# Kernel optimization log

Measured on AMD Instinct MI355X. Metric: run time of the kernel, lower is better.

Reference implementation:

```python
import jax, jax.numpy as jnp
import numpy as np

N, E, F_IN, NHID, HEADS, NGRAPHS = 50000, 800000, 128, 256, 4, 16
C = NHID // HEADS          # 64 per-head channels
NEG_SLOPE = 0.2            # PyG GATConv default negative_slope


def setup_inputs() -> dict:
    key = jax.random.key(0)
    k = jax.random.split(key, 7)
    x = jax.random.normal(k[0], (N, F_IN), jnp.float32)
    edge_index = jax.random.randint(k[1], (2, E), 0, N)          # [2, E] src/dst
    batch = jnp.sort(jax.random.randint(k[2], (N,), 0, NGRAPHS))  # node -> graph id
    # learned params of GATConv(F_IN, C, heads=HEADS), concat=True
    W = jax.random.normal(k[3], (F_IN, NHID), jnp.float32) / np.sqrt(F_IN)
    att_src = jax.random.normal(k[4], (HEADS, C), jnp.float32) * 0.1
    att_dst = jax.random.normal(k[5], (HEADS, C), jnp.float32) * 0.1
    bias = jax.random.normal(k[6], (NHID,), jnp.float32) * 0.01
    return {"x": x, "edge_index": edge_index, "batch": batch,
            "W": W, "att_src": att_src, "att_dst": att_dst, "bias": bias}


def _segment_softmax(logits, seg, num_segments):
    # softmax over all edges sharing the same destination node
    m = jax.ops.segment_max(logits, seg, num_segments=num_segments)
    m = jnp.where(jnp.isfinite(m), m, jnp.zeros_like(m))  # guard empty segments
    e = jnp.exp(logits - m[seg])
    s = jax.ops.segment_sum(e, seg, num_segments=num_segments)
    return e / (s[seg] + 1e-16)


def reference(x, edge_index, batch, W, att_src, att_dst, bias):
    n = x.shape[0]
    # PyG GATConv adds self-loops by default
    loops = jnp.arange(n, dtype=edge_index.dtype)
    src = jnp.concatenate([edge_index[0], loops])
    dst = jnp.concatenate([edge_index[1], loops])
    xp = (x @ W).reshape(n, HEADS, C)                       # [N, H, C]
    a_src = jnp.einsum('nhc,hc->nh', xp, att_src)           # [N, H]
    a_dst = jnp.einsum('nhc,hc->nh', xp, att_dst)
    logits = jax.nn.leaky_relu(a_src[src] + a_dst[dst], NEG_SLOPE)  # [E+N, H]
    alpha = _segment_softmax(logits, dst, n)
    msg = xp[src] * alpha[:, :, None]                       # [E+N, H, C]
    out = jax.ops.segment_sum(msg, dst, num_segments=n).reshape(n, NHID) + bias
    h = jax.nn.relu(out)                                    # hidden_act='relu'
    # global max / mean pooling per graph, then concat
    gmax = jax.ops.segment_max(h, batch, num_segments=NGRAPHS)
    cnt = jax.ops.segment_sum(jnp.ones((n, 1), h.dtype), batch, num_segments=NGRAPHS)
    gmean = jax.ops.segment_sum(h, batch, num_segments=NGRAPHS) / (cnt + 1e-16)
    return jnp.concatenate([gmax, gmean], axis=1)           # [NGRAPHS, 2*NHID]
```

## Files before the change

### kernel.cpp

```cpp
#include <hip/hip_runtime.h>

#define NN 50000
#define NE 800000
#define FIN 128
#define NHID 256
#define HEADS 4
#define CPH 64
#define NG 16
#define ETOT (NE + NN)
#define NEG_SLOPE 0.2f
#define MAXDEG 64

__device__ __forceinline__ float lrelu(float x) {
    return x > 0.f ? x : NEG_SLOPE * x;
}
__device__ __forceinline__ unsigned short bf16_rne(float f) {
    unsigned u = __float_as_uint(f);
    unsigned r = (u + 0x7fffu + ((u >> 16) & 1u)) >> 16;
    return (unsigned short)r;
}
__device__ __forceinline__ float bf16_to_f(unsigned short h) {
    return __uint_as_float((unsigned)h << 16);
}
__device__ __forceinline__ float bf16_lo(unsigned u) {
    return __uint_as_float(u << 16);
}
__device__ __forceinline__ float bf16_hi(unsigned u) {
    return __uint_as_float(u & 0xffff0000u);
}

using frag_ab = __attribute__((ext_vector_type(8))) short;
using frag_cd = __attribute__((ext_vector_type(4))) float;

__global__ __launch_bounds__(256) void k_scatter(const int* __restrict__ ei,
                                                 const float* __restrict__ W,
                                                 unsigned short* __restrict__ Wt16,
                                                 int* __restrict__ deg,
                                                 unsigned short* __restrict__ elist) {
    int bid = blockIdx.x;
    if (bid < 128) {
        int idx = bid * 256 + threadIdx.x;
        int n = idx >> 7;
        int k = idx & 127;
        Wt16[idx] = bf16_rne(W[(size_t)k * NHID + n]);
        return;
    }
    int e = (bid - 128) * 256 + threadIdx.x;
    if (e >= ETOT) return;
    int s, d;
    if (e < NE) { s = ei[e]; d = ei[NE + e]; } else { s = d = e - NE; }
    int pos = atomicAdd(&deg[d], 1);
    if (pos < MAXDEG) elist[d * MAXDEG + pos] = (unsigned short)s;
}

__global__ __launch_bounds__(256) void k_gemm(const float* __restrict__ x,
                                              const unsigned short* __restrict__ Wt16,
                                              const float* __restrict__ att_src,
                                              const float* __restrict__ att_dst,
                                              unsigned short* __restrict__ xp16,
                                              float* __restrict__ a_src,
                                              float* __restrict__ a_dst) {
    __shared__ __align__(16) unsigned short smem[64 * 264];
    const int tid = threadIdx.x;
    const int row0 = blockIdx.x * 64;

    {
        int r = tid >> 2;
        int c0 = (tid & 3) * 32;
        int gr = row0 + r;
        if (gr < NN) {
            #pragma unroll
            for (int i = 0; i < 8; i++) {
                float4 v = *(const float4*)&x[(size_t)gr * FIN + c0 + i * 4];
                ushort4 o;
                o.x = bf16_rne(v.x); o.y = bf16_rne(v.y);
                o.z = bf16_rne(v.z); o.w = bf16_rne(v.w);
                *(ushort4*)&smem[r * 264 + c0 + i * 4] = o;
            }
        } else {
            ushort4 z = {0, 0, 0, 0};
            #pragma unroll
            for (int i = 0; i < 8; i++) *(ushort4*)&smem[r * 264 + c0 + i * 4] = z;
        }
    }
    __syncthreads();

    const int wv = tid >> 6;
    const int lane = tid & 63;
    const int rowhalf = wv >> 1;
    const int colhalf = wv & 1;
    const int m = lane & 15;
    const int q = lane >> 4;
    const int cbase = colhalf * 128;

    frag_cd acc[2][8];
    #pragma unroll
    for (int rt = 0; rt < 2; rt++)
        #pragma unroll
        for (int c = 0; c < 8; c++)
            acc[rt][c] = (frag_cd){0.f, 0.f, 0.f, 0.f};

    #pragma unroll
    for (int k0 = 0; k0 < FIN; k0 += 32) {
        frag_ab af0 = *(const frag_ab*)&smem[(rowhalf * 32 + m) * 264 + k0 + q * 8];
        frag_ab af1 = *(const frag_ab*)&smem[(rowhalf * 32 + 16 + m) * 264 + k0 + q * 8];
        #pragma unroll
        for (int c = 0; c < 8; c++) {
            int n = cbase + c * 16 + m;
            frag_ab bf = *(const frag_ab*)&Wt16[(size_t)n * FIN + k0 + q * 8];
            acc[0][c] = __builtin_amdgcn_mfma_f32_16x16x32_bf16(af0, bf, acc[0][c], 0, 0, 0);
            acc[1][c] = __builtin_amdgcn_mfma_f32_16x16x32_bf16(af1, bf, acc[1][c], 0, 0, 0);
        }
    }

    float asv[8], adv[8];
    #pragma unroll
    for (int c = 0; c < 8; c++) {
        asv[c] = att_src[cbase + c * 16 + m];
        adv[c] = att_dst[cbase + c * 16 + m];
    }
    const int headA = colhalf * 2;
    const int headB = colhalf * 2 + 1;

    #pragma unroll
    for (int rt = 0; rt < 2; rt++) {
        #pragma unroll
        for (int reg = 0; reg < 4; reg++) {
            int grow = row0 + rowhalf * 32 + rt * 16 + q * 4 + reg;
            bool ok = grow < NN;
            float psA = 0.f, psB = 0.f, pdA = 0.f, pdB = 0.f;
            #pragma unroll
            for (int c = 0; c < 4; c++) {
                psA += acc[rt][c][reg] * asv[c];
                pdA += acc[rt][c][reg] * adv[c];
                psB += acc[rt][c + 4][reg] * asv[c + 4];
                pdB += acc[rt][c + 4][reg] * adv[c + 4];
            }
            #pragma unroll
            for (int off = 1; off < 16; off <<= 1) {
                psA += __shfl_xor(psA, off, 64);
                psB += __shfl_xor(psB, off, 64);
                pdA += __shfl_xor(pdA, off, 64);
                pdB += __shfl_xor(pdB, off, 64);
            }
            if (m == 0 && ok) {
                a_src[grow * 4 + headA] = psA;
                a_src[grow * 4 + headB] = psB;
                a_dst[grow * 4 + headA] = pdA;
                a_dst[grow * 4 + headB] = pdB;
            }
        }
    }

    __syncthreads();
    #pragma unroll
    for (int rt = 0; rt < 2; rt++)
        #pragma unroll
        for (int c = 0; c < 8; c++)
            #pragma unroll
            for (int reg = 0; reg < 4; reg++)
                smem[(rowhalf * 32 + rt * 16 + q * 4 + reg) * 264 + cbase + c * 16 + m] =
                    bf16_rne(acc[rt][c][reg]);
    __syncthreads();
    {
        int r = tid >> 2;
        int cg = (tid & 3) * 64;
        int gr = row0 + r;
        if (gr < NN) {
            #pragma unroll
            for (int j = 0; j < 2; j++) {
                uint4 v0 = *(const uint4*)&smem[r * 264 + cg + j * 32];
                uint4 v1 = *(const uint4*)&smem[r * 264 + cg + j * 32 + 8];
                uint4 v2 = *(const uint4*)&smem[r * 264 + cg + j * 32 + 16];
                uint4 v3 = *(const uint4*)&smem[r * 264 + cg + j * 32 + 24];
                *(uint4*)&xp16[(size_t)gr * NHID + cg + j * 32] = v0;
                *(uint4*)&xp16[(size_t)gr * NHID + cg + j * 32 + 8] = v1;
                *(uint4*)&xp16[(size_t)gr * NHID + cg + j * 32 + 16] = v2;
                *(uint4*)&xp16[(size_t)gr * NHID + cg + j * 32 + 24] = v3;
            }
        }
    }
}

__global__ __launch_bounds__(256) void k_agg(const unsigned short* __restrict__ elist,
                                             const int* __restrict__ deg,
                                             const float* __restrict__ a_src,
                                             const float* __restrict__ a_dst,
                                             const unsigned short* __restrict__ xp16,
                                             const float* __restrict__ bias,
                                             unsigned short* __restrict__ hbuf16) {
    __shared__ float wlds[4][MAXDEG][4];
    __shared__ int   slds[4][MAXDEG];
    int wv = threadIdx.x >> 6;
    int lane = threadIdx.x & 63;
    int d = blockIdx.x * 4 + wv;
    if (d >= NN) return;
    int dg = deg[d]; if (dg > MAXDEG) dg = MAXDEG;

    float4 ad = *(const float4*)&a_dst[d * 4];

    float4 lg = make_float4(-1e30f, -1e30f, -1e30f, -1e30f);
    if (lane < dg) {
        int s = elist[d * MAXDEG + lane];
        slds[wv][lane] = s;
        float4 as = *(const float4*)&a_src[s * 4];
        lg.x = lrelu(as.x + ad.x);
        lg.y = lrelu(as.y + ad.y);
        lg.z = lrelu(as.z + ad.z);
        lg.w = lrelu(as.w + ad.w);
    }
    float4 m = lg;
    #pragma unroll
    for (int off = 1; off < 64; off <<= 1) {
        m.x = fmaxf(m.x, __shfl_xor(m.x, off, 64));
        m.y = fmaxf(m.y, __shfl_xor(m.y, off, 64));
        m.z = fmaxf(m.z, __shfl_xor(m.z, off, 64));
        m.w = fmaxf(m.w, __shfl_xor(m.w, off, 64));
    }
    float4 w = make_float4(0.f, 0.f, 0.f, 0.f);
    if (lane < dg) {
        w.x = expf(lg.x - m.x);
        w.y = expf(lg.y - m.y);
        w.z = expf(lg.z - m.z);
        w.w = expf(lg.w - m.w);
    }
    *(float4*)&wlds[wv][lane][0] = w;
    float4 sm = w;
    #pragma unroll
    for (int off = 1; off < 64; off <<= 1) {
        sm.x += __shfl_xor(sm.x, off, 64);
        sm.y += __shfl_xor(sm.y, off, 64);
        sm.z += __shfl_xor(sm.z, off, 64);
        sm.w += __shfl_xor(sm.w, off, 64);
    }

    const int half = lane >> 5;
    const int hl = lane & 31;
    const int ch0 = hl * 8;
    const int hh = hl >> 3;
    float denom = (hh == 0 ? sm.x : hh == 1 ? sm.y : hh == 2 ? sm.z : sm.w) + 1e-16f;

    float acc0[8] = {}, acc1[8] = {};
    int e = half;
    for (; e + 2 < dg; e += 4) {
        int sA = slds[wv][e];
        int sB = slds[wv][e + 2];
        float wA = wlds[wv][e][hh];
        float wB = wlds[wv][e + 2][hh];
        uint4 uA = *(const uint4*)&xp16[(size_t)sA * NHID + ch0];
        uint4 uB = *(const uint4*)&xp16[(size_t)sB * NHID + ch0];
        acc0[0] += wA * bf16_lo(uA.x); acc0[1] += wA * bf16_hi(uA.x);
        acc0[2] += wA * bf16_lo(uA.y); acc0[3] += wA * bf16_hi(uA.y);
        acc0[4] += wA * bf16_lo(uA.z); acc0[5] += wA * bf16_hi(uA.z);
        acc0[6] += wA * bf16_lo(uA.w); acc0[7] += wA * bf16_hi(uA.w);
        acc1[0] += wB * bf16_lo(uB.x); acc1[1] += wB * bf16_hi(uB.x);
        acc1[2] += wB * bf16_lo(uB.y); acc1[3] += wB * bf16_hi(uB.y);
        acc1[4] += wB * bf16_lo(uB.z); acc1[5] += wB * bf16_hi(uB.z);
        acc1[6] += wB * bf16_lo(uB.w); acc1[7] += wB * bf16_hi(uB.w);
    }
    if (e < dg) {
        int sA = slds[wv][e];
        float wA = wlds[wv][e][hh];
        uint4 uA = *(const uint4*)&xp16[(size_t)sA * NHID + ch0];
        acc0[0] += wA * bf16_lo(uA.x); acc0[1] += wA * bf16_hi(uA.x);
        acc0[2] += wA * bf16_lo(uA.y); acc0[3] += wA * bf16_hi(uA.y);
        acc0[4] += wA * bf16_lo(uA.z); acc0[5] += wA * bf16_hi(uA.z);
        acc0[6] += wA * bf16_lo(uA.w); acc0[7] += wA * bf16_hi(uA.w);
    }
    #pragma unroll
    for (int j = 0; j < 8; j++) {
        acc0[j] += acc1[j];
        acc0[j] += __shfl_xor(acc0[j], 32, 64);
    }
    if (half == 0) {
        float4 b1 = *(const float4*)&bias[ch0];
        float4 b2 = *(const float4*)&bias[ch0 + 4];
        ushort4 oA, oB;
        oA.x = bf16_rne(fmaxf(acc0[0] / denom + b1.x, 0.f));
        oA.y = bf16_rne(fmaxf(acc0[1] / denom + b1.y, 0.f));
        oA.z = bf16_rne(fmaxf(acc0[2] / denom + b1.z, 0.f));
        oA.w = bf16_rne(fmaxf(acc0[3] / denom + b1.w, 0.f));
        oB.x = bf16_rne(fmaxf(acc0[4] / denom + b2.x, 0.f));
        oB.y = bf16_rne(fmaxf(acc0[5] / denom + b2.y, 0.f));
        oB.z = bf16_rne(fmaxf(acc0[6] / denom + b2.z, 0.f));
        oB.w = bf16_rne(fmaxf(acc0[7] / denom + b2.w, 0.f));
        *(ushort4*)&hbuf16[(size_t)d * NHID + ch0] = oA;
        *(ushort4*)&hbuf16[(size_t)d * NHID + ch0 + 4] = oB;
    }
}

#define NPB 128
__global__ __launch_bounds__(256) void k_pool(const unsigned short* __restrict__ hbuf16,
                                              const int* __restrict__ batch,
                                              float* __restrict__ gmax,
                                              float* __restrict__ gsum) {
    int c = threadIdx.x;
    int n0 = blockIdx.x * NPB;
    if (n0 >= NN) return;
    float lmax = 0.f, lsum = 0.f;
    int cur_g = batch[n0];
    int nend = n0 + NPB; if (nend > NN) nend = NN;
    for (int n = n0; n < nend; n++) {
        int g = batch[n];
        if (g != cur_g) {
            atomicMax((int*)&gmax[cur_g * NHID + c], __float_as_int(lmax));
            atomicAdd(&gsum[cur_g * NHID + c], lsum);
            lmax = 0.f; lsum = 0.f; cur_g = g;
        }
        float val = bf16_to_f(hbuf16[(size_t)n * NHID + c]);
        lmax = fmaxf(lmax, val);
        lsum += val;
    }
    atomicMax((int*)&gmax[cur_g * NHID + c], __float_as_int(lmax));
    atomicAdd(&gsum[cur_g * NHID + c], lsum);
}

__device__ __forceinline__ int lb_batch(const int* __restrict__ batch, int val) {
    int lo = 0, hi = NN;
    while (lo < hi) {
        int mid = (lo + hi) >> 1;
        if (batch[mid] < val) lo = mid + 1; else hi = mid;
    }
    return lo;
}

__global__ __launch_bounds__(512) void k_final(const float* __restrict__ gmax,
                                               const float* __restrict__ gsum,
                                               const int* __restrict__ batch,
                                               float* __restrict__ out) {
    __shared__ float inv_cnt;
    int g = blockIdx.x;
    if (threadIdx.x == 0) {
        int lo = lb_batch(batch, g);
        int hi = lb_batch(batch, g + 1);
        inv_cnt = 1.0f / ((float)(hi - lo) + 1e-16f);
    }
    __syncthreads();
    int j = threadIdx.x;
    float v;
    if (j < 256) v = gmax[g * NHID + j];
    else v = gsum[g * NHID + (j - 256)] * inv_cnt;
    out[g * 512 + j] = v;
}

extern "C" void kernel_launch(void* const* d_in, const int* in_sizes, int n_in,
                              void* d_out, int out_size, void* d_ws, size_t ws_size,
                              hipStream_t stream) {
    const float* x      = (const float*)d_in[0];
    const int*   ei     = (const int*)d_in[1];
    const int*   batch  = (const int*)d_in[2];
    const float* W      = (const float*)d_in[3];
    const float* attS   = (const float*)d_in[4];
    const float* attD   = (const float*)d_in[5];
    const float* bias   = (const float*)d_in[6];
    float* out = (float*)d_out;

    float* ws = (float*)d_ws;
    unsigned short* xp16   = (unsigned short*)ws;
    float*          a_src  = (float*)(xp16 + (size_t)NN * NHID + 256);
    float*          a_dst  = a_src + 200000;
    unsigned short* hbuf16 = (unsigned short*)(a_dst + 200000);
    unsigned short* elist  = hbuf16 + (size_t)NN * NHID;
    int*            deg    = (int*)(elist + (size_t)NN * MAXDEG);
    float*          gmax   = (float*)(deg + NN);
    float*          gsum   = gmax + 4096;
    unsigned short* Wt16   = (unsigned short*)(gsum + 4096);

    size_t zero_bytes = (size_t)(NN + 4096 + 4096) * 4;
    hipMemsetAsync((void*)deg, 0, zero_bytes, stream);

    k_scatter<<<128 + (ETOT + 255) / 256, 256, 0, stream>>>(ei, W, Wt16, deg, elist);
    k_gemm<<<(NN + 63) / 64, 256, 0, stream>>>(x, Wt16, attS, attD, xp16, a_src, a_dst);
    k_agg<<<(NN + 3) / 4, 256, 0, stream>>>(elist, deg, a_src, a_dst, xp16, bias, hbuf16);
    k_pool<<<(NN + NPB - 1) / NPB, 256, 0, stream>>>(hbuf16, batch, gmax, gsum);
    k_final<<<NG, 512, 0, stream>>>(gmax, gsum, batch, out);
}
```

Measured before the change: 273.4 us.

## Fuse scatter, GEMM and zeroing into one front kernel; merge pool and final

Merges the edge-scatter, GEMM and workspace zeroing into one launch, splitting the work by block ID. The GEMM now reads fp32 W directly and converts it to bf16 on the fly, so the separate W transpose pass goes away. Pool and final are merged through a last-block counter with atomic reads. The aggregation softmax drops its max-subtraction, which removes two shuffle reductions but risks exp overflow for large logits. This cuts launches and memsets, but the strided uncoalesced W loads in the GEMM inner loop may cost more than they save.

After: 321.7 us. 17.7% more time.

```diff
diff --git a/kernel.cpp b/kernel.cpp
--- a/kernel.cpp
+++ b/kernel.cpp
@@ -5,12 +5,17 @@
 #define FIN 128
 #define NHID 256
 #define HEADS 4
-#define CPH 64
 #define NG 16
 #define ETOT (NE + NN)
 #define NEG_SLOPE 0.2f
 #define MAXDEG 64
 
+#define ZB 8
+#define NBS ((ETOT + 255) / 256)
+#define NBG ((NN + 63) / 64)
+#define NPB 128
+#define NBP ((NN + NPB - 1) / NPB)
+
 __device__ __forceinline__ float lrelu(float x) {
     return x > 0.f ? x : NEG_SLOPE * x;
 }
@@ -32,37 +37,37 @@
 using frag_ab = __attribute__((ext_vector_type(8))) short;
 using frag_cd = __attribute__((ext_vector_type(4))) float;
 
-__global__ __launch_bounds__(256) void k_scatter(const int* __restrict__ ei,
-                                                 const float* __restrict__ W,
-                                                 unsigned short* __restrict__ Wt16,
-                                                 int* __restrict__ deg,
-                                                 unsigned short* __restrict__ elist) {
-    int bid = blockIdx.x;
-    if (bid < 128) {
-        int idx = bid * 256 + threadIdx.x;
-        int n = idx >> 7;
-        int k = idx & 127;
-        Wt16[idx] = bf16_rne(W[(size_t)k * NHID + n]);
+__global__ __launch_bounds__(256) void k_front(const float* __restrict__ x,
+                                               const float* __restrict__ W,
+                                               const float* __restrict__ att_src,
+                                               const float* __restrict__ att_dst,
+                                               const int* __restrict__ ei,
+                                               int* __restrict__ deg,
+                                               unsigned short* __restrict__ elist,
+                                               unsigned short* __restrict__ xp16,
+                                               float* __restrict__ a_src,
+                                               float* __restrict__ a_dst,
+                                               float* __restrict__ zbase) {
+    __shared__ __align__(16) unsigned short smem[64 * 264];
+    const int bid = blockIdx.x;
+    const int tid = threadIdx.x;
+
+    if (bid < ZB) {
+        for (int i = bid * 256 + tid; i < 4096 + 4096 + 1; i += ZB * 256)
+            zbase[i] = 0.f;
         return;
     }
-    int e = (bid - 128) * 256 + threadIdx.x;
-    if (e >= ETOT) return;
-    int s, d;
-    if (e < NE) { s = ei[e]; d = ei[NE + e]; } else { s = d = e - NE; }
-    int pos = atomicAdd(&deg[d], 1);
-    if (pos < MAXDEG) elist[d * MAXDEG + pos] = (unsigned short)s;
-}
-
-__global__ __launch_bounds__(256) void k_gemm(const float* __restrict__ x,
-                                              const unsigned short* __restrict__ Wt16,
-                                              const float* __restrict__ att_src,
-                                              const float* __restrict__ att_dst,
-                                              unsigned short* __restrict__ xp16,
-                                              float* __restrict__ a_src,
-                                              float* __restrict__ a_dst) {
-    __shared__ __align__(16) unsigned short smem[64 * 264];
-    const int tid = threadIdx.x;
-    const int row0 = blockIdx.x * 64;
+    if (bid < ZB + NBS) {
+        int e = (bid - ZB) * 256 + tid;
+        if (e >= ETOT) return;
+        int s, d;
+        if (e < NE) { s = ei[e]; d = ei[NE + e]; } else { s = d = e - NE; }
+        int pos = atomicAdd(&deg[d], 1);
+        if (pos < MAXDEG) elist[d * MAXDEG + pos] = (unsigned short)s;
+        return;
+    }
+
+    const int row0 = (bid - ZB - NBS) * 64;
 
     {
         int r = tid >> 2;
@@ -107,7 +112,11 @@
         #pragma unroll
         for (int c = 0; c < 8; c++) {
             int n = cbase + c * 16 + m;
-            frag_ab bf = *(const frag_ab*)&Wt16[(size_t)n * FIN + k0 + q * 8];
+            const float* wp = &W[(size_t)(k0 + q * 8) * NHID + n];
+            frag_ab bf;
+            #pragma unroll
+            for (int j = 0; j < 8; j++)
+                bf[j] = (short)bf16_rne(wp[(size_t)j * NHID]);
             acc[0][c] = __builtin_amdgcn_mfma_f32_16x16x32_bf16(af0, bf, acc[0][c], 0, 0, 0);
             acc[1][c] = __builtin_amdgcn_mfma_f32_16x16x32_bf16(af1, bf, acc[1][c], 0, 0, 0);
         }
@@ -199,30 +208,15 @@
 
     float4 ad = *(const float4*)&a_dst[d * 4];
 
-    float4 lg = make_float4(-1e30f, -1e30f, -1e30f, -1e30f);
+    float4 w = make_float4(0.f, 0.f, 0.f, 0.f);
     if (lane < dg) {
         int s = elist[d * MAXDEG + lane];
         slds[wv][lane] = s;
         float4 as = *(const float4*)&a_src[s * 4];
-        lg.x = lrelu(as.x + ad.x);
-        lg.y = lrelu(as.y + ad.y);
-        lg.z = lrelu(as.z + ad.z);
-        lg.w = lrelu(as.w + ad.w);
-    }
-    float4 m = lg;
-    #pragma unroll
-    for (int off = 1; off < 64; off <<= 1) {
-        m.x = fmaxf(m.x, __shfl_xor(m.x, off, 64));
-        m.y = fmaxf(m.y, __shfl_xor(m.y, off, 64));
-        m.z = fmaxf(m.z, __shfl_xor(m.z, off, 64));
-        m.w = fmaxf(m.w, __shfl_xor(m.w, off, 64));
-    }
-    float4 w = make_float4(0.f, 0.f, 0.f, 0.f);
-    if (lane < dg) {
-        w.x = expf(lg.x - m.x);
-        w.y = expf(lg.y - m.y);
-        w.z = expf(lg.z - m.z);
-        w.w = expf(lg.w - m.w);
+        w.x = expf(lrelu(as.x + ad.x));
+        w.y = expf(lrelu(as.y + ad.y));
+        w.z = expf(lrelu(as.z + ad.z));
+        w.w = expf(lrelu(as.w + ad.w));
     }
     *(float4*)&wlds[wv][lane][0] = w;
     float4 sm = w;
@@ -289,32 +283,6 @@
     }
 }
 
-#define NPB 128
-__global__ __launch_bounds__(256) void k_pool(const unsigned short* __restrict__ hbuf16,
-                                              const int* __restrict__ batch,
-                                              float* __restrict__ gmax,
-                                              float* __restrict__ gsum) {
-    int c = threadIdx.x;
-    int n0 = blockIdx.x * NPB;
-    if (n0 >= NN) return;
-    float lmax = 0.f, lsum = 0.f;
-    int cur_g = batch[n0];
-    int nend = n0 + NPB; if (nend > NN) nend = NN;
-    for (int n = n0; n < nend; n++) {
-        int g = batch[n];
-        if (g != cur_g) {
-            atomicMax((int*)&gmax[cur_g * NHID + c], __float_as_int(lmax));
-            atomicAdd(&gsum[cur_g * NHID + c], lsum);
-            lmax = 0.f; lsum = 0.f; cur_g = g;
-        }
-        float val = bf16_to_f(hbuf16[(size_t)n * NHID + c]);
-        lmax = fmaxf(lmax, val);
-        lsum += val;
-    }
-    atomicMax((int*)&gmax[cur_g * NHID + c], __float_as_int(lmax));
-    atomicAdd(&gsum[cur_g * NHID + c], lsum);
-}
-
 __device__ __forceinline__ int lb_batch(const int* __restrict__ batch, int val) {
     int lo = 0, hi = NN;
     while (lo < hi) {
@@ -324,23 +292,59 @@
     return lo;
 }
 
-__global__ __launch_bounds__(512) void k_final(const float* __restrict__ gmax,
-                                               const float* __restrict__ gsum,
-                                               const int* __restrict__ batch,
-                                               float* __restrict__ out) {
-    __shared__ float inv_cnt;
-    int g = blockIdx.x;
-    if (threadIdx.x == 0) {
-        int lo = lb_batch(batch, g);
-        int hi = lb_batch(batch, g + 1);
-        inv_cnt = 1.0f / ((float)(hi - lo) + 1e-16f);
-    }
-    __syncthreads();
-    int j = threadIdx.x;
-    float v;
-    if (j < 256) v = gmax[g * NHID + j];
-    else v = gsum[g * NHID + (j - 256)] * inv_cnt;
-    out[g * 512 + j] = v;
+__global__ __launch_bounds__(256) void k_poolfinal(const unsigned short* __restrict__ hbuf16,
+                                                   const int* __restrict__ batch,
+                                                   float* __restrict__ gmax,
+                                                   float* __restrict__ gsum,
+                                                   int* __restrict__ counter,
+                                                   float* __restrict__ out) {
+    const int c = threadIdx.x;
+    const int n0 = blockIdx.x * NPB;
+    if (n0 < NN) {
+        float lmax = 0.f, lsum = 0.f;
+        int cur_g = batch[n0];
+        int nend = n0 + NPB; if (nend > NN) nend = NN;
+        for (int n = n0; n < nend; n++) {
+            int g = batch[n];
+            if (g != cur_g) {
+                atomicMax((int*)&gmax[cur_g * NHID + c], __float_as_int(lmax));
+                atomicAdd(&gsum[cur_g * NHID + c], lsum);
+                lmax = 0.f; lsum = 0.f; cur_g = g;
+            }
+            float val = bf16_to_f(hbuf16[(size_t)n * NHID + c]);
+            lmax = fmaxf(lmax, val);
+            lsum += val;
+        }
+        atomicMax((int*)&gmax[cur_g * NHID + c], __float_as_int(lmax));
+        atomicAdd(&gsum[cur_g * NHID + c], lsum);
+    }
+
+    __shared__ int is_last;
+    __threadfence();
+    __syncthreads();
+    if (c == 0) {
+        int old = atomicAdd(counter, 1);
+        is_last = (old == (int)gridDim.x - 1);
+    }
+    __syncthreads();
+    if (!is_last) return;
+    __threadfence();
+
+    __shared__ float invc[NG];
+    if (c < NG) {
+        int lo = lb_batch(batch, c);
+        int hi = lb_batch(batch, c + 1);
+        invc[c] = 1.0f / ((float)(hi - lo) + 1e-16f);
+    }
+    __syncthreads();
+    for (int i = c; i < NG * 512; i += 256) {
+        int g = i >> 9;
+        int j = i & 511;
+        float v;
+        if (j < 256) v = __int_as_float(atomicMax((int*)&gmax[g * NHID + j], 0));
+        else v = atomicAdd(&gsum[g * NHID + (j - 256)], 0.0f) * invc[g];
+        out[i] = v;
+    }
 }
 
 extern "C" void kernel_launch(void* const* d_in, const int* in_sizes, int n_in,
@@ -362,16 +366,15 @@
     unsigned short* hbuf16 = (unsigned short*)(a_dst + 200000);
     unsigned short* elist  = hbuf16 + (size_t)NN * NHID;
     int*            deg    = (int*)(elist + (size_t)NN * MAXDEG);
-    float*          gmax   = (float*)(deg + NN);
+    float*          zbase  = (float*)(deg + NN);
+    float*          gmax   = zbase;
     float*          gsum   = gmax + 4096;
-    unsigned short* Wt16   = (unsigned short*)(gsum + 4096);
-
-    size_t zero_bytes = (size_t)(NN + 4096 + 4096) * 4;
-    hipMemsetAsync((void*)deg, 0, zero_bytes, stream);
-
-    k_scatter<<<128 + (ETOT + 255) / 256, 256, 0, stream>>>(ei, W, Wt16, deg, elist);
-    k_gemm<<<(NN + 63) / 64, 256, 0, stream>>>(x, Wt16, attS, attD, xp16, a_src, a_dst);
+    int*            counter = (int*)(gsum + 4096);
+
+    hipMemsetAsync((void*)deg, 0, (size_t)NN * 4, stream);
+
+    k_front<<<ZB + NBS + NBG, 256, 0, stream>>>(x, W, attS, attD, ei, deg, elist,
+                                                xp16, a_src, a_dst, zbase);
     k_agg<<<(NN + 3) / 4, 256, 0, stream>>>(elist, deg, a_src, a_dst, xp16, bias, hbuf16);
-    k_pool<<<(NN + NPB - 1) / NPB, 256, 0, stream>>>(hbuf16, batch, gmax, gsum);
-    k_final<<<NG, 512, 0, stream>>>(gmax, gsum, batch, out);
-}
+    k_poolfinal<<<NBP, 256, 0, stream>>>(hbuf16, batch, gmax, gsum, counter, out);
+}
```
